# Optimization experiments

Hardware: AMD Instinct MI355X
Metric: run time of the kernel (lower is better)

The kernel has to match this reference:

```python
import jax, jax.numpy as jnp
import numpy as np
from jax.ops import segment_sum, segment_max

IN_CH, HID, OUT_CH, HEADS = 128, 64, 32, 4
N_NODES, N_EDGES = 50000, 800000
NEG_SLOPE = 0.2
EPS = 1e-16


def gat_layer(x, edge_index, W, att_src, att_dst, bias, heads, out_ch, concat):
    """PyG-style GATConv (add_self_loops=False, dropout=0, no edge features)."""
    N = x.shape[0]
    src, dst = edge_index[0], edge_index[1]
    h = (x @ W).reshape(N, heads, out_ch)                 # [N, H, C]
    a_src = jnp.einsum('nhc,hc->nh', h, att_src)          # [N, H]
    a_dst = jnp.einsum('nhc,hc->nh', h, att_dst)          # [N, H]
    e = jax.nn.leaky_relu(a_src[src] + a_dst[dst], NEG_SLOPE)  # [E, H]
    # segment softmax over incoming edges of each dst node
    m = segment_max(e, dst, num_segments=N)               # [N, H]
    ex = jnp.exp(e - m[dst])                              # [E, H]
    s = segment_sum(ex, dst, num_segments=N)              # [N, H]
    alpha = ex / (s[dst] + EPS)                           # [E, H]
    msg = h[src] * alpha[..., None]                       # [E, H, C]
    out = segment_sum(msg, dst, num_segments=N)           # [N, H, C]
    if concat:
        out = out.reshape(N, heads * out_ch)
    else:
        out = out.mean(axis=1)
    return out + bias, alpha


def setup_inputs() -> dict:
    key = jax.random.key(0)
    ks = jax.random.split(key, 10)
    s_in = 1.0 / np.sqrt(IN_CH)
    s_h = 1.0 / np.sqrt(HEADS * HID)
    return {
        'x': jax.random.normal(ks[0], (N_NODES, IN_CH), jnp.float32),
        'edge_index': jax.random.randint(ks[1], (2, N_EDGES), 0, N_NODES, jnp.int32),
        'W1': jax.random.normal(ks[2], (IN_CH, HEADS * HID), jnp.float32) * s_in,
        'att_src1': jax.random.normal(ks[3], (HEADS, HID), jnp.float32) * s_h,
        'att_dst1': jax.random.normal(ks[4], (HEADS, HID), jnp.float32) * s_h,
        'bias1': jnp.zeros((HEADS * HID,), jnp.float32),
        'W2': jax.random.normal(ks[5], (HEADS * HID, OUT_CH), jnp.float32) * s_h,
        'att_src2': jax.random.normal(ks[6], (1, OUT_CH), jnp.float32) * s_h,
        'att_dst2': jax.random.normal(ks[7], (1, OUT_CH), jnp.float32) * s_h,
        'bias2': jnp.zeros((OUT_CH,), jnp.float32),
    }


def reference(x, edge_index, W1, att_src1, att_dst1, bias1, W2, att_src2, att_dst2, bias2):
    h1, alpha1 = gat_layer(x, edge_index, W1, att_src1, att_dst1, bias1, HEADS, HID, concat=True)
    h1 = jax.nn.elu(h1)
    h2, alpha2 = gat_layer(h1, edge_index, W2, att_src2, att_dst2, bias2, 1, OUT_CH, concat=False)
    return h2, edge_index, alpha1, edge_index, alpha2
```

## Files before the change

### kernel.cpp

```cpp
#include <hip/hip_runtime.h>
#include <hip/hip_fp16.h>
#include <math.h>

#define NEG_SLOPE 0.2f
#define EPS_C 1e-16f

typedef _Float16 f16x8 __attribute__((ext_vector_type(8)));
typedef float f32x4 __attribute__((ext_vector_type(4)));

__device__ __forceinline__ float lrelu(float x){ return x > 0.f ? x : NEG_SLOPE * x; }
__device__ __forceinline__ float eluf(float x){ return x > 0.f ? x : expm1f(x); }

__global__ void zero_int_kernel(int* __restrict__ p, int n){
  int i = blockIdx.x * blockDim.x + threadIdx.x;
  if (i < n) p[i] = 0;
}

__global__ void count_deg_kernel(const int* __restrict__ dst, int* __restrict__ deg, int E){
  int i = blockIdx.x * blockDim.x + threadIdx.x;
  if (i < E) atomicAdd(&deg[dst[i]], 1);
}

__global__ __launch_bounds__(256) void scan1_kernel(const int* __restrict__ deg,
    int* __restrict__ offsets, int* __restrict__ blockSums, int N){
  __shared__ int sm[256];
  int b = blockIdx.x, t = threadIdx.x;
  int i = b * 256 + t;
  int v = (i < N) ? deg[i] : 0;
  sm[t] = v;
  __syncthreads();
  #pragma unroll
  for (int st = 1; st < 256; st <<= 1){
    int add = (t >= st) ? sm[t - st] : 0;
    __syncthreads();
    sm[t] += add;
    __syncthreads();
  }
  if (i < N) offsets[i] = sm[t] - v;
  if (t == 255) blockSums[b] = sm[255];
}

__global__ __launch_bounds__(256) void scan2_kernel(const int* __restrict__ blockSums,
    int* __restrict__ blockBase, int* __restrict__ offsetsN, int nb){
  __shared__ int sm[256];
  int t = threadIdx.x;
  int v = (t < nb) ? blockSums[t] : 0;
  sm[t] = v;
  __syncthreads();
  #pragma unroll
  for (int st = 1; st < 256; st <<= 1){
    int add = (t >= st) ? sm[t - st] : 0;
    __syncthreads();
    sm[t] += add;
    __syncthreads();
  }
  if (t < nb) blockBase[t] = sm[t] - v;
  if (t == 255) *offsetsN = sm[255];
}

__global__ __launch_bounds__(256) void scan3_kernel(int* __restrict__ offsets,
    const int* __restrict__ blockBase, int* __restrict__ cursor, int N){
  int b = blockIdx.x, t = threadIdx.x;
  int i = b * 256 + t;
  if (i < N){
    int v = offsets[i] + blockBase[b];
    offsets[i] = v;
    cursor[i] = v;
  }
}

__global__ void scatter_kernel(const int* __restrict__ src, const int* __restrict__ dst,
                               int* __restrict__ cursor, int* __restrict__ csr_src,
                               int* __restrict__ csr_eid, int E){
  int i = blockIdx.x * blockDim.x + threadIdx.x;
  if (i < E){
    int d = dst[i];
    int p = atomicAdd(&cursor[d], 1);
    csr_src[p] = src[i];
    csr_eid[p] = i;
  }
}

__global__ void cvt_x_kernel(const float* __restrict__ x, __half* __restrict__ x16, int n4){
  int i = blockIdx.x * blockDim.x + threadIdx.x;
  if (i < n4){
    float4 v = *reinterpret_cast<const float4*>(&x[(size_t)i * 4]);
    __half2 h01 = __floats2half2_rn(v.x, v.y);
    __half2 h23 = __floats2half2_rn(v.z, v.w);
    uint2 pack;
    pack.x = *reinterpret_cast<unsigned int*>(&h01);
    pack.y = *reinterpret_cast<unsigned int*>(&h23);
    *reinterpret_cast<uint2*>(&x16[(size_t)i * 4]) = pack;
  }
}

__global__ void cvt_w1_kernel(const float* __restrict__ W1, __half* __restrict__ W1t){
  int i = blockIdx.x * blockDim.x + threadIdx.x;
  int k = i >> 8, c = i & 255;
  if (i < 128 * 256) W1t[(size_t)c * 128 + k] = __float2half(W1[(size_t)k * 256 + c]);
}

__global__ __launch_bounds__(256) void gemm1_kernel(const __half* __restrict__ x16,
    const __half* __restrict__ W1t, const float* __restrict__ att_src,
    const float* __restrict__ att_dst, __half* __restrict__ h1,
    float* __restrict__ a_src_f, float* __restrict__ a_dst_f, int N){
  __shared__ _Float16 As[128 * 136];
  __shared__ _Float16 Bs[64 * 136];
  int tid = threadIdx.x;
  int lane = tid & 63, wid = tid >> 6;
  int rowBase = blockIdx.x * 128;
  int head = blockIdx.y;
  int colBase = head * 64;

  #pragma unroll
  for (int it = 0; it < 8; ++it){
    int li = it * 256 + tid;
    int r = li >> 4, seg = li & 15;
    int grow = rowBase + r;
    f16x8 v = {};
    if (grow < N) v = *reinterpret_cast<const f16x8*>(&x16[(size_t)grow * 128 + seg * 8]);
    *reinterpret_cast<f16x8*>(&As[r * 136 + seg * 8]) = v;
  }
  #pragma unroll
  for (int it = 0; it < 4; ++it){
    int li = it * 256 + tid;
    int c = li >> 4, seg = li & 15;
    f16x8 v = *reinterpret_cast<const f16x8*>(&W1t[(size_t)(colBase + c) * 128 + seg * 8]);
    *reinterpret_cast<f16x8*>(&Bs[c * 136 + seg * 8]) = v;
  }
  __syncthreads();

  f32x4 acc[2][4] = {};
  int l15 = lane & 15, l4 = lane >> 4;
  #pragma unroll
  for (int ks = 0; ks < 4; ++ks){
    int kOff = ks * 32 + l4 * 8;
    f16x8 a0 = *reinterpret_cast<const f16x8*>(&As[(wid * 32 + l15) * 136 + kOff]);
    f16x8 a1 = *reinterpret_cast<const f16x8*>(&As[(wid * 32 + 16 + l15) * 136 + kOff]);
    #pragma unroll
    for (int cc = 0; cc < 4; ++cc){
      f16x8 b = *reinterpret_cast<const f16x8*>(&Bs[(cc * 16 + l15) * 136 + kOff]);
      acc[0][cc] = __builtin_amdgcn_mfma_f32_16x16x32_f16(a0, b, acc[0][cc], 0, 0, 0);
      acc[1][cc] = __builtin_amdgcn_mfma_f32_16x16x32_f16(a1, b, acc[1][cc], 0, 0, 0);
    }
  }

  #pragma unroll
  for (int rr = 0; rr < 2; ++rr){
    #pragma unroll
    for (int i = 0; i < 4; ++i){
      int row = rowBase + wid * 32 + rr * 16 + l4 * 4 + i;
      if (row < N){
        #pragma unroll
        for (int cc = 0; cc < 4; ++cc)
          h1[(size_t)row * 256 + colBase + cc * 16 + l15] = __float2half(acc[rr][cc][i]);
      }
    }
  }
  float sw[4], dw[4];
  #pragma unroll
  for (int cc = 0; cc < 4; ++cc){
    sw[cc] = att_src[colBase + cc * 16 + l15];
    dw[cc] = att_dst[colBase + cc * 16 + l15];
  }
  #pragma unroll
  for (int rr = 0; rr < 2; ++rr){
    #pragma unroll
    for (int i = 0; i < 4; ++i){
      float ts = 0.f, td = 0.f;
      #pragma unroll
      for (int cc = 0; cc < 4; ++cc){
        ts += acc[rr][cc][i] * sw[cc];
        td += acc[rr][cc][i] * dw[cc];
      }
      #pragma unroll
      for (int st = 8; st > 0; st >>= 1){
        ts += __shfl_xor(ts, st);
        td += __shfl_xor(td, st);
      }
      int row = rowBase + wid * 32 + rr * 16 + l4 * 4 + i;
      if (l15 == 0 && row < N){
        a_src_f[(size_t)row * 4 + head] = ts;
        a_dst_f[(size_t)row * 4 + head] = td;
      }
    }
  }
}

__global__ __launch_bounds__(256) void node1_kernel(
    const __half* __restrict__ h1, const float4* __restrict__ a_src,
    const float* __restrict__ a_src_f, const float4* __restrict__ a_dst,
    const int* __restrict__ offsets, const int* __restrict__ csr_src,
    const int* __restrict__ csr_eid, const float* __restrict__ bias,
    float* __restrict__ h1b, float* __restrict__ alpha1_out, int N){
  int gid = blockIdx.x * blockDim.x + threadIdx.x;
  int n = gid >> 6, lane = gid & 63;
  if (n >= N) return;
  int off = offsets[n];
  int deg = offsets[n + 1] - off;
  float4 ad = a_dst[n];
  bool have0 = (lane < deg);
  float4 e0 = make_float4(-INFINITY, -INFINITY, -INFINITY, -INFINITY);
  if (have0){
    float4 as = a_src[csr_src[off + lane]];
    e0 = make_float4(lrelu(as.x + ad.x), lrelu(as.y + ad.y),
                     lrelu(as.z + ad.z), lrelu(as.w + ad.w));
  }
  float m0 = e0.x, m1 = e0.y, m2 = e0.z, m3 = e0.w;
  for (int i = lane + 64; i < deg; i += 64){
    float4 as = a_src[csr_src[off + i]];
    m0 = fmaxf(m0, lrelu(as.x + ad.x));
    m1 = fmaxf(m1, lrelu(as.y + ad.y));
    m2 = fmaxf(m2, lrelu(as.z + ad.z));
    m3 = fmaxf(m3, lrelu(as.w + ad.w));
  }
  #pragma unroll
  for (int st = 32; st > 0; st >>= 1){
    m0 = fmaxf(m0, __shfl_xor(m0, st));
    m1 = fmaxf(m1, __shfl_xor(m1, st));
    m2 = fmaxf(m2, __shfl_xor(m2, st));
    m3 = fmaxf(m3, __shfl_xor(m3, st));
  }
  float s0 = 0.f, s1 = 0.f, s2 = 0.f, s3 = 0.f;
  if (have0){
    s0 = __expf(e0.x - m0); s1 = __expf(e0.y - m1);
    s2 = __expf(e0.z - m2); s3 = __expf(e0.w - m3);
  }
  for (int i = lane + 64; i < deg; i += 64){
    float4 as = a_src[csr_src[off + i]];
    s0 += __expf(lrelu(as.x + ad.x) - m0);
    s1 += __expf(lrelu(as.y + ad.y) - m1);
    s2 += __expf(lrelu(as.z + ad.z) - m2);
    s3 += __expf(lrelu(as.w + ad.w) - m3);
  }
  #pragma unroll
  for (int st = 32; st > 0; st >>= 1){
    s0 += __shfl_xor(s0, st); s1 += __shfl_xor(s1, st);
    s2 += __shfl_xor(s2, st); s3 += __shfl_xor(s3, st);
  }
  float i0 = 1.f / (s0 + EPS_C), i1 = 1.f / (s1 + EPS_C);
  float i2 = 1.f / (s2 + EPS_C), i3 = 1.f / (s3 + EPS_C);
  if (have0){
    int eid = csr_eid[off + lane];
    *reinterpret_cast<float4*>(&alpha1_out[(size_t)eid * 4]) =
        make_float4(__expf(e0.x - m0) * i0, __expf(e0.y - m1) * i1,
                    __expf(e0.z - m2) * i2, __expf(e0.w - m3) * i3);
  }
  for (int i = lane + 64; i < deg; i += 64){
    int slot = off + i;
    float4 as = a_src[csr_src[slot]];
    int eid = csr_eid[slot];
    *reinterpret_cast<float4*>(&alpha1_out[(size_t)eid * 4]) =
        make_float4(__expf(lrelu(as.x + ad.x) - m0) * i0,
                    __expf(lrelu(as.y + ad.y) - m1) * i1,
                    __expf(lrelu(as.z + ad.z) - m2) * i2,
                    __expf(lrelu(as.w + ad.w) - m3) * i3);
  }
  int head = lane >> 4;
  float mh  = head == 0 ? m0 : head == 1 ? m1 : head == 2 ? m2 : m3;
  float ih  = head == 0 ? i0 : head == 1 ? i1 : head == 2 ? i2 : i3;
  float adh = head == 0 ? ad.x : head == 1 ? ad.y : head == 2 ? ad.z : ad.w;
  float4 accA = make_float4(0.f, 0.f, 0.f, 0.f);
  float4 accB = make_float4(0.f, 0.f, 0.f, 0.f);
  float4 accC = make_float4(0.f, 0.f, 0.f, 0.f);
  float4 accD = make_float4(0.f, 0.f, 0.f, 0.f);
  int j = 0;
  for (; j + 3 < deg; j += 4){
    int sA = csr_src[off + j];
    int sB = csr_src[off + j + 1];
    int sC = csr_src[off + j + 2];
    int sD = csr_src[off + j + 3];
    float alA = __expf(lrelu(a_src_f[(size_t)sA * 4 + head] + adh) - mh) * ih;
    float alB = __expf(lrelu(a_src_f[(size_t)sB * 4 + head] + adh) - mh) * ih;
    float alC = __expf(lrelu(a_src_f[(size_t)sC * 4 + head] + adh) - mh) * ih;
    float alD = __expf(lrelu(a_src_f[(size_t)sD * 4 + head] + adh) - mh) * ih;
    float2 rA = *reinterpret_cast<const float2*>(&h1[(size_t)sA * 256 + lane * 4]);
    float2 rB = *reinterpret_cast<const float2*>(&h1[(size_t)sB * 256 + lane * 4]);
    float2 rC = *reinterpret_cast<const float2*>(&h1[(size_t)sC * 256 + lane * 4]);
    float2 rD = *reinterpret_cast<const float2*>(&h1[(size_t)sD * 256 + lane * 4]);
    float2 fA0 = __half22float2(*reinterpret_cast<__half2*>(&rA.x));
    float2 fA1 = __half22float2(*reinterpret_cast<__half2*>(&rA.y));
    float2 fB0 = __half22float2(*reinterpret_cast<__half2*>(&rB.x));
    float2 fB1 = __half22float2(*reinterpret_cast<__half2*>(&rB.y));
    float2 fC0 = __half22float2(*reinterpret_cast<__half2*>(&rC.x));
    float2 fC1 = __half22float2(*reinterpret_cast<__half2*>(&rC.y));
    float2 fD0 = __half22float2(*reinterpret_cast<__half2*>(&rD.x));
    float2 fD1 = __half22float2(*reinterpret_cast<__half2*>(&rD.y));
    accA.x += alA * fA0.x; accA.y += alA * fA0.y; accA.z += alA * fA1.x; accA.w += alA * fA1.y;
    accB.x += alB * fB0.x; accB.y += alB * fB0.y; accB.z += alB * fB1.x; accB.w += alB * fB1.y;
    accC.x += alC * fC0.x; accC.y += alC * fC0.y; accC.z += alC * fC1.x; accC.w += alC * fC1.y;
    accD.x += alD * fD0.x; accD.y += alD * fD0.y; accD.z += alD * fD1.x; accD.w += alD * fD1.y;
  }
  for (; j < deg; ++j){
    int sA = csr_src[off + j];
    float alA = __expf(lrelu(a_src_f[(size_t)sA * 4 + head] + adh) - mh) * ih;
    float2 rA = *reinterpret_cast<const float2*>(&h1[(size_t)sA * 256 + lane * 4]);
    float2 fA0 = __half22float2(*reinterpret_cast<__half2*>(&rA.x));
    float2 fA1 = __half22float2(*reinterpret_cast<__half2*>(&rA.y));
    accA.x += alA * fA0.x; accA.y += alA * fA0.y; accA.z += alA * fA1.x; accA.w += alA * fA1.y;
  }
  accA.x += accB.x + accC.x + accD.x;
  accA.y += accB.y + accC.y + accD.y;
  accA.z += accB.z + accC.z + accD.z;
  accA.w += accB.w + accC.w + accD.w;
  float4 b = *reinterpret_cast<const float4*>(&bias[lane * 4]);
  float4 o = make_float4(eluf(accA.x + b.x), eluf(accA.y + b.y),
                         eluf(accA.z + b.z), eluf(accA.w + b.w));
  *reinterpret_cast<float4*>(&h1b[(size_t)n * 256 + lane * 4]) = o;
}

__global__ __launch_bounds__(256) void gemm2_kernel(const float* __restrict__ h1b,
    const float* __restrict__ W2, const float* __restrict__ att_src2,
    const float* __restrict__ att_dst2, float* __restrict__ h2pre,
    float* __restrict__ a_src2, float* __restrict__ a_dst2, int N){
  __shared__ float As[128][33];
  __shared__ float Bs[32][33];
  int tid = threadIdx.x;
  int tx = tid & 15, ty = tid >> 4;
  int rowBase = blockIdx.x * 128;
  float acc[8][2] = {};
  float4 pa[4], pb;

  #pragma unroll
  for (int it = 0; it < 4; ++it){
    int li = it * 256 + tid;
    int r = li >> 3, kk = (li & 7) << 2;
    int row = rowBase + r;
    pa[it] = (row < N) ? *reinterpret_cast<const float4*>(&h1b[(size_t)row * 256 + kk])
                       : make_float4(0.f, 0.f, 0.f, 0.f);
  }
  {
    int kr = tid >> 3, c4 = (tid & 7) << 2;
    pb = *reinterpret_cast<const float4*>(&W2[(size_t)kr * 32 + c4]);
  }
  #pragma unroll
  for (int it = 0; it < 4; ++it){
    int li = it * 256 + tid;
    int r = li >> 3, kk = (li & 7) << 2;
    As[r][kk] = pa[it].x; As[r][kk + 1] = pa[it].y;
    As[r][kk + 2] = pa[it].z; As[r][kk + 3] = pa[it].w;
  }
  {
    int kr = tid >> 3, c4 = (tid & 7) << 2;
    Bs[kr][c4] = pb.x; Bs[kr][c4 + 1] = pb.y; Bs[kr][c4 + 2] = pb.z; Bs[kr][c4 + 3] = pb.w;
  }
  __syncthreads();

  for (int k0 = 0; k0 < 256; k0 += 32){
    bool more = (k0 + 32) < 256;
    if (more){
      #pragma unroll
      for (int it = 0; it < 4; ++it){
        int li = it * 256 + tid;
        int r = li >> 3, kk = (li & 7) << 2;
        int row = rowBase + r;
        pa[it] = (row < N) ? *reinterpret_cast<const float4*>(&h1b[(size_t)row * 256 + k0 + 32 + kk])
                           : make_float4(0.f, 0.f, 0.f, 0.f);
      }
      int kr = tid >> 3, c4 = (tid & 7) << 2;
      pb = *reinterpret_cast<const float4*>(&W2[(size_t)(k0 + 32 + kr) * 32 + c4]);
    }
    #pragma unroll
    for (int kk = 0; kk < 32; ++kk){
      float b0 = Bs[kk][tx * 2], b1 = Bs[kk][tx * 2 + 1];
      #pragma unroll
      for (int j = 0; j < 8; ++j){
        float a = As[ty + 16 * j][kk];
        acc[j][0] += a * b0; acc[j][1] += a * b1;
      }
    }
    if (more){
      __syncthreads();
      #pragma unroll
      for (int it = 0; it < 4; ++it){
        int li = it * 256 + tid;
        int r = li >> 3, kk = (li & 7) << 2;
        As[r][kk] = pa[it].x; As[r][kk + 1] = pa[it].y;
        As[r][kk + 2] = pa[it].z; As[r][kk + 3] = pa[it].w;
      }
      int kr = tid >> 3, c4 = (tid & 7) << 2;
      Bs[kr][c4] = pb.x; Bs[kr][c4 + 1] = pb.y; Bs[kr][c4 + 2] = pb.z; Bs[kr][c4 + 3] = pb.w;
      __syncthreads();
    }
  }
  #pragma unroll
  for (int j = 0; j < 8; ++j){
    int row = rowBase + ty + 16 * j;
    if (row < N)
      *reinterpret_cast<float2*>(&h2pre[(size_t)row * 32 + tx * 2]) =
          make_float2(acc[j][0], acc[j][1]);
  }
  float s0 = att_src2[tx * 2], s1 = att_src2[tx * 2 + 1];
  float d0 = att_dst2[tx * 2], d1 = att_dst2[tx * 2 + 1];
  float ps[8], pd[8];
  #pragma unroll
  for (int j = 0; j < 8; ++j){
    ps[j] = acc[j][0] * s0 + acc[j][1] * s1;
    pd[j] = acc[j][0] * d0 + acc[j][1] * d1;
  }
  #pragma unroll
  for (int st = 8; st > 0; st >>= 1){
    #pragma unroll
    for (int j = 0; j < 8; ++j){
      ps[j] += __shfl_xor(ps[j], st);
      pd[j] += __shfl_xor(pd[j], st);
    }
  }
  if (tx == 0){
    #pragma unroll
    for (int j = 0; j < 8; ++j){
      int row = rowBase + ty + 16 * j;
      if (row < N){
        a_src2[row] = ps[j];
        a_dst2[row] = pd[j];
      }
    }
  }
}

__global__ __launch_bounds__(256) void node2_kernel(
    const float* __restrict__ h2pre, const float* __restrict__ a_src2,
    const float* __restrict__ a_dst2, const int* __restrict__ offsets,
    const int* __restrict__ csr_src, const int* __restrict__ csr_eid,
    const float* __restrict__ bias2, float* __restrict__ out_h2,
    float* __restrict__ alpha2_out, int N){
  int gid = blockIdx.x * blockDim.x + threadIdx.x;
  int n = gid >> 6, lane = gid & 63;
  if (n >= N) return;
  int off = offsets[n], deg = offsets[n + 1] - off;
  float adn = a_dst2[n];
  bool have0 = (lane < deg);
  float e0 = -INFINITY;
  if (have0) e0 = lrelu(a_src2[csr_src[off + lane]] + adn);
  float m = e0;
  for (int i = lane + 64; i < deg; i += 64)
    m = fmaxf(m, lrelu(a_src2[csr_src[off + i]] + adn));
  #pragma unroll
  for (int st = 32; st > 0; st >>= 1) m = fmaxf(m, __shfl_xor(m, st));
  float s = have0 ? __expf(e0 - m) : 0.f;
  for (int i = lane + 64; i < deg; i += 64)
    s += __expf(lrelu(a_src2[csr_src[off + i]] + adn) - m);
  #pragma unroll
  for (int st = 32; st > 0; st >>= 1) s += __shfl_xor(s, st);
  float inv = 1.f / (s + EPS_C);
  if (have0) alpha2_out[csr_eid[off + lane]] = __expf(e0 - m) * inv;
  for (int i = lane + 64; i < deg; i += 64){
    int slot = off + i;
    alpha2_out[csr_eid[slot]] = __expf(lrelu(a_src2[csr_src[slot]] + adn) - m) * inv;
  }
  int c = lane & 31, half = lane >> 5;
  float acc = 0.f;
  for (int j = half; j < deg; j += 2){
    int src = csr_src[off + j];
    float al = __expf(lrelu(a_src2[src] + adn) - m) * inv;
    acc += al * h2pre[(size_t)src * 32 + c];
  }
  acc += __shfl_xor(acc, 32);
  if (lane < 32) out_h2[(size_t)n * 32 + c] = acc + bias2[c];
}

__global__ void edge_out_kernel(const int* __restrict__ ei, float* __restrict__ out1,
                                float* __restrict__ out3, int n2e){
  int i = blockIdx.x * blockDim.x + threadIdx.x;
  if (i < n2e){
    float v = (float)ei[i];
    out1[i] = v; out3[i] = v;
  }
}

extern "C" void kernel_launch(void* const* d_in, const int* in_sizes, int n_in,
                              void* d_out, int out_size, void* d_ws, size_t ws_size,
                              hipStream_t stream){
  const float* x        = (const float*)d_in[0];
  const int*   ei       = (const int*)d_in[1];
  const float* W1       = (const float*)d_in[2];
  const float* att_src1 = (const float*)d_in[3];
  const float* att_dst1 = (const float*)d_in[4];
  const float* bias1    = (const float*)d_in[5];
  const float* W2       = (const float*)d_in[6];
  const float* att_src2 = (const float*)d_in[7];
  const float* att_dst2 = (const float*)d_in[8];
  const float* bias2    = (const float*)d_in[9];
  float* out = (float*)d_out;
  (void)n_in; (void)out_size; (void)ws_size;

  const int N = in_sizes[0] / 128;
  const int E = in_sizes[1] / 2;
  const int* src = ei;
  const int* dst = ei + E;
  const int nb = (N + 255) / 256;

  char* ws = (char*)d_ws;
  size_t o = 0;
  auto alloc = [&](size_t bytes) -> void* {
    void* p = ws + o;
    o += (bytes + 255) & ~(size_t)255;
    return p;
  };
  __half* h1      = (__half*)alloc((size_t)N * 256 * 2);
  __half* x16     = (__half*)alloc((size_t)N * 128 * 2);
  __half* W1t     = (__half*)alloc((size_t)256 * 128 * 2);
  float*  h1b     = (float*)alloc((size_t)N * 256 * 4);
  float*  h2pre   = (float*)alloc((size_t)N * 32 * 4);
  float*  a_src1  = (float*)alloc((size_t)N * 16);
  float*  a_dst1  = (float*)alloc((size_t)N * 16);
  float*  a_src2  = (float*)alloc((size_t)N * 4);
  float*  a_dst2  = (float*)alloc((size_t)N * 4);
  int*    deg     = (int*)alloc((size_t)N * 4);
  int*    offsets = (int*)alloc((size_t)(N + 1) * 4);
  int*    cursor  = (int*)alloc((size_t)N * 4);
  int*    csr_src = (int*)alloc((size_t)E * 4);
  int*    csr_eid = (int*)alloc((size_t)E * 4);
  int*    blockSums = (int*)alloc(256 * 4);
  int*    blockBase = (int*)alloc(256 * 4);

  const size_t OFF1 = (size_t)N * 32;
  const size_t OFF2 = OFF1 + (size_t)2 * E;
  const size_t OFF3 = OFF2 + (size_t)E * 4;
  const size_t OFF4 = OFF3 + (size_t)2 * E;

  int n4 = (N * 128) / 4;
  hipLaunchKernelGGL(cvt_x_kernel, dim3((n4 + 255) / 256), dim3(256), 0, stream, x, x16, n4);
  hipLaunchKernelGGL(cvt_w1_kernel, dim3(128), dim3(256), 0, stream, W1, W1t);
  hipLaunchKernelGGL(zero_int_kernel, dim3((N + 255) / 256), dim3(256), 0, stream, deg, N);
  hipLaunchKernelGGL(count_deg_kernel, dim3((E + 255) / 256), dim3(256), 0, stream, dst, deg, E);
  hipLaunchKernelGGL(scan1_kernel, dim3(nb), dim3(256), 0, stream, deg, offsets, blockSums, N);
  hipLaunchKernelGGL(scan2_kernel, dim3(1), dim3(256), 0, stream, blockSums, blockBase,
                     offsets + N, nb);
  hipLaunchKernelGGL(scan3_kernel, dim3(nb), dim3(256), 0, stream, offsets, blockBase, cursor, N);
  hipLaunchKernelGGL(scatter_kernel, dim3((E + 255) / 256), dim3(256), 0, stream,
                     src, dst, cursor, csr_src, csr_eid, E);
  hipLaunchKernelGGL(gemm1_kernel, dim3((N + 127) / 128, 4), dim3(256), 0, stream,
                     x16, W1t, att_src1, att_dst1, h1, a_src1, a_dst1, N);
  hipLaunchKernelGGL(node1_kernel, dim3((N * 64 + 255) / 256), dim3(256), 0, stream,
                     h1, (const float4*)a_src1, (const float*)a_src1, (const float4*)a_dst1,
                     offsets, csr_src, csr_eid, bias1, h1b, out + OFF2, N);
  hipLaunchKernelGGL(gemm2_kernel, dim3((N + 127) / 128), dim3(256), 0, stream,
                     h1b, W2, att_src2, att_dst2, h2pre, a_src2, a_dst2, N);
  hipLaunchKernelGGL(node2_kernel, dim3((N * 64 + 255) / 256), dim3(256), 0, stream,
                     h2pre, a_src2, a_dst2, offsets, csr_src, csr_eid, bias2,
                     out, out + OFF4, N);
  hipLaunchKernelGGL(edge_out_kernel, dim3((2 * E + 255) / 256), dim3(256), 0, stream,
                     ei, out + OFF1, out + OFF3, 2 * E);
}
```

Measured before the change: 389.9 us.

## Store layer-1 output in fp16, use MFMA for GEMM2, cache alphas in LDS

The post-ELU hidden activations and the second-layer projection are now stored as fp16 instead of fp32, halving their memory traffic. GEMM2 is rewritten around fp16 MFMA using a transposed fp16 copy of W2. Both node kernels keep the per-edge attention coefficients of the first 64 edges in LDS, so the aggregation loops no longer re-gather a_src and recompute the exponentials. The cost is reduced precision in the intermediate activations plus one extra tiny conversion kernel.

```diff
diff --git a/kernel.cpp b/kernel.cpp
--- a/kernel.cpp
+++ b/kernel.cpp
@@ -98,6 +98,12 @@
   int i = blockIdx.x * blockDim.x + threadIdx.x;
   int k = i >> 8, c = i & 255;
   if (i < 128 * 256) W1t[(size_t)c * 128 + k] = __float2half(W1[(size_t)k * 256 + c]);
+}
+
+__global__ void cvt_w2_kernel(const float* __restrict__ W2, __half* __restrict__ W2t){
+  int i = blockIdx.x * blockDim.x + threadIdx.x;
+  int k = i >> 5, c = i & 31;
+  if (i < 256 * 32) W2t[(size_t)c * 256 + k] = __float2half(W2[(size_t)k * 32 + c]);
 }
 
 __global__ __launch_bounds__(256) void gemm1_kernel(const __half* __restrict__ x16,
@@ -192,9 +198,10 @@
     const float* __restrict__ a_src_f, const float4* __restrict__ a_dst,
     const int* __restrict__ offsets, const int* __restrict__ csr_src,
     const int* __restrict__ csr_eid, const float* __restrict__ bias,
-    float* __restrict__ h1b, float* __restrict__ alpha1_out, int N){
+    __half* __restrict__ h1b, float* __restrict__ alpha1_out, int N){
+  __shared__ float al_lds[4][4][64];
   int gid = blockIdx.x * blockDim.x + threadIdx.x;
-  int n = gid >> 6, lane = gid & 63;
+  int n = gid >> 6, lane = gid & 63, wid = (threadIdx.x >> 6) & 3;
   if (n >= N) return;
   int off = offsets[n];
   int deg = offsets[n + 1] - off;
@@ -241,10 +248,12 @@
   float i0 = 1.f / (s0 + EPS_C), i1 = 1.f / (s1 + EPS_C);
   float i2 = 1.f / (s2 + EPS_C), i3 = 1.f / (s3 + EPS_C);
   if (have0){
+    float a0 = __expf(e0.x - m0) * i0, a1 = __expf(e0.y - m1) * i1;
+    float a2 = __expf(e0.z - m2) * i2, a3 = __expf(e0.w - m3) * i3;
+    al_lds[wid][0][lane] = a0; al_lds[wid][1][lane] = a1;
+    al_lds[wid][2][lane] = a2; al_lds[wid][3][lane] = a3;
     int eid = csr_eid[off + lane];
-    *reinterpret_cast<float4*>(&alpha1_out[(size_t)eid * 4]) =
-        make_float4(__expf(e0.x - m0) * i0, __expf(e0.y - m1) * i1,
-                    __expf(e0.z - m2) * i2, __expf(e0.w - m3) * i3);
+    *reinterpret_cast<float4*>(&alpha1_out[(size_t)eid * 4]) = make_float4(a0, a1, a2, a3);
   }
   for (int i = lane + 64; i < deg; i += 64){
     int slot = off + i;
@@ -264,16 +273,17 @@
   float4 accB = make_float4(0.f, 0.f, 0.f, 0.f);
   float4 accC = make_float4(0.f, 0.f, 0.f, 0.f);
   float4 accD = make_float4(0.f, 0.f, 0.f, 0.f);
+  int degL = deg < 64 ? deg : 64;
   int j = 0;
-  for (; j + 3 < deg; j += 4){
+  for (; j + 3 < degL; j += 4){
     int sA = csr_src[off + j];
     int sB = csr_src[off + j + 1];
     int sC = csr_src[off + j + 2];
     int sD = csr_src[off + j + 3];
-    float alA = __expf(lrelu(a_src_f[(size_t)sA * 4 + head] + adh) - mh) * ih;
-    float alB = __expf(lrelu(a_src_f[(size_t)sB * 4 + head] + adh) - mh) * ih;
-    float alC = __expf(lrelu(a_src_f[(size_t)sC * 4 + head] + adh) - mh) * ih;
-    float alD = __expf(lrelu(a_src_f[(size_t)sD * 4 + head] + adh) - mh) * ih;
+    float alA = al_lds[wid][head][j];
+    float alB = al_lds[wid][head][j + 1];
+    float alC = al_lds[wid][head][j + 2];
+    float alD = al_lds[wid][head][j + 3];
     float2 rA = *reinterpret_cast<const float2*>(&h1[(size_t)sA * 256 + lane * 4]);
     float2 rB = *reinterpret_cast<const float2*>(&h1[(size_t)sB * 256 + lane * 4]);
     float2 rC = *reinterpret_cast<const float2*>(&h1[(size_t)sC * 256 + lane * 4]);
@@ -291,6 +301,14 @@
     accC.x += alC * fC0.x; accC.y += alC * fC0.y; accC.z += alC * fC1.x; accC.w += alC * fC1.y;
     accD.x += alD * fD0.x; accD.y += alD * fD0.y; accD.z += alD * fD1.x; accD.w += alD * fD1.y;
   }
+  for (; j < degL; ++j){
+    int sA = csr_src[off + j];
+    float alA = al_lds[wid][head][j];
+    float2 rA = *reinterpret_cast<const float2*>(&h1[(size_t)sA * 256 + lane * 4]);
+    float2 fA0 = __half22float2(*reinterpret_cast<__half2*>(&rA.x));
+    float2 fA1 = __half22float2(*reinterpret_cast<__half2*>(&rA.y));
+    accA.x += alA * fA0.x; accA.y += alA * fA0.y; accA.z += alA * fA1.x; accA.w += alA * fA1.y;
+  }
   for (; j < deg; ++j){
     int sA = csr_src[off + j];
     float alA = __expf(lrelu(a_src_f[(size_t)sA * 4 + head] + adh) - mh) * ih;
@@ -304,128 +322,101 @@
   accA.z += accB.z + accC.z + accD.z;
   accA.w += accB.w + accC.w + accD.w;
   float4 b = *reinterpret_cast<const float4*>(&bias[lane * 4]);
-  float4 o = make_float4(eluf(accA.x + b.x), eluf(accA.y + b.y),
-                         eluf(accA.z + b.z), eluf(accA.w + b.w));
-  *reinterpret_cast<float4*>(&h1b[(size_t)n * 256 + lane * 4]) = o;
-}
-
-__global__ __launch_bounds__(256) void gemm2_kernel(const float* __restrict__ h1b,
-    const float* __restrict__ W2, const float* __restrict__ att_src2,
-    const float* __restrict__ att_dst2, float* __restrict__ h2pre,
+  __half2 o01 = __floats2half2_rn(eluf(accA.x + b.x), eluf(accA.y + b.y));
+  __half2 o23 = __floats2half2_rn(eluf(accA.z + b.z), eluf(accA.w + b.w));
+  uint2 pack;
+  pack.x = *reinterpret_cast<unsigned int*>(&o01);
+  pack.y = *reinterpret_cast<unsigned int*>(&o23);
+  *reinterpret_cast<uint2*>(&h1b[(size_t)n * 256 + lane * 4]) = pack;
+}
+
+__global__ __launch_bounds__(256) void gemm2_kernel(const __half* __restrict__ h1b,
+    const __half* __restrict__ W2t, const float* __restrict__ att_src2,
+    const float* __restrict__ att_dst2, __half* __restrict__ h2pre,
     float* __restrict__ a_src2, float* __restrict__ a_dst2, int N){
-  __shared__ float As[128][33];
-  __shared__ float Bs[32][33];
+  __shared__ _Float16 As[128 * 136];
+  __shared__ _Float16 Bs[32 * 136];
   int tid = threadIdx.x;
-  int tx = tid & 15, ty = tid >> 4;
+  int lane = tid & 63, wid = tid >> 6;
   int rowBase = blockIdx.x * 128;
-  float acc[8][2] = {};
-  float4 pa[4], pb;
-
-  #pragma unroll
-  for (int it = 0; it < 4; ++it){
-    int li = it * 256 + tid;
-    int r = li >> 3, kk = (li & 7) << 2;
-    int row = rowBase + r;
-    pa[it] = (row < N) ? *reinterpret_cast<const float4*>(&h1b[(size_t)row * 256 + kk])
-                       : make_float4(0.f, 0.f, 0.f, 0.f);
-  }
-  {
-    int kr = tid >> 3, c4 = (tid & 7) << 2;
-    pb = *reinterpret_cast<const float4*>(&W2[(size_t)kr * 32 + c4]);
-  }
-  #pragma unroll
-  for (int it = 0; it < 4; ++it){
-    int li = it * 256 + tid;
-    int r = li >> 3, kk = (li & 7) << 2;
-    As[r][kk] = pa[it].x; As[r][kk + 1] = pa[it].y;
-    As[r][kk + 2] = pa[it].z; As[r][kk + 3] = pa[it].w;
-  }
-  {
-    int kr = tid >> 3, c4 = (tid & 7) << 2;
-    Bs[kr][c4] = pb.x; Bs[kr][c4 + 1] = pb.y; Bs[kr][c4 + 2] = pb.z; Bs[kr][c4 + 3] = pb.w;
-  }
-  __syncthreads();
-
-  for (int k0 = 0; k0 < 256; k0 += 32){
-    bool more = (k0 + 32) < 256;
-    if (more){
+  int l15 = lane & 15, l4 = lane >> 4;
+  f32x4 acc[2][2] = {};
+
+  for (int kc = 0; kc < 2; ++kc){
+    if (kc) __syncthreads();
+    #pragma unroll
+    for (int it = 0; it < 8; ++it){
+      int li = it * 256 + tid;
+      int r = li >> 4, seg = li & 15;
+      int grow = rowBase + r;
+      f16x8 v = {};
+      if (grow < N) v = *reinterpret_cast<const f16x8*>(&h1b[(size_t)grow * 256 + kc * 128 + seg * 8]);
+      *reinterpret_cast<f16x8*>(&As[r * 136 + seg * 8]) = v;
+    }
+    #pragma unroll
+    for (int it = 0; it < 2; ++it){
+      int li = it * 256 + tid;
+      int c = li >> 4, seg = li & 15;
+      f16x8 v = *reinterpret_cast<const f16x8*>(&W2t[(size_t)c * 256 + kc * 128 + seg * 8]);
+      *reinterpret_cast<f16x8*>(&Bs[c * 136 + seg * 8]) = v;
+    }
+    __syncthreads();
+    #pragma unroll
+    for (int ks = 0; ks < 4; ++ks){
+      int kOff = ks * 32 + l4 * 8;
+      f16x8 a0 = *reinterpret_cast<const f16x8*>(&As[(wid * 32 + l15) * 136 + kOff]);
+      f16x8 a1 = *reinterpret_cast<const f16x8*>(&As[(wid * 32 + 16 + l15) * 136 + kOff]);
       #pragma unroll
-      for (int it = 0; it < 4; ++it){
-        int li = it * 256 + tid;
-        int r = li >> 3, kk = (li & 7) << 2;
-        int row = rowBase + r;
-        pa[it] = (row < N) ? *reinterpret_cast<const float4*>(&h1b[(size_t)row * 256 + k0 + 32 + kk])
-                           : make_float4(0.f, 0.f, 0.f, 0.f);
-      }
-      int kr = tid >> 3, c4 = (tid & 7) << 2;
-      pb = *reinterpret_cast<const float4*>(&W2[(size_t)(k0 + 32 + kr) * 32 + c4]);
-    }
-    #pragma unroll
-    for (int kk = 0; kk < 32; ++kk){
-      float b0 = Bs[kk][tx * 2], b1 = Bs[kk][tx * 2 + 1];
+      for (int cb = 0; cb < 2; ++cb){
+        f16x8 b = *reinterpret_cast<const f16x8*>(&Bs[(cb * 16 + l15) * 136 + kOff]);
+        acc[0][cb] = __builtin_amdgcn_mfma_f32_16x16x32_f16(a0, b, acc[0][cb], 0, 0, 0);
+        acc[1][cb] = __builtin_amdgcn_mfma_f32_16x16x32_f16(a1, b, acc[1][cb], 0, 0, 0);
+      }
+    }
+  }
+  #pragma unroll
+  for (int rr = 0; rr < 2; ++rr){
+    #pragma unroll
+    for (int i = 0; i < 4; ++i){
+      int row = rowBase + wid * 32 + rr * 16 + l4 * 4 + i;
+      if (row < N){
+        #pragma unroll
+        for (int cb = 0; cb < 2; ++cb)
+          h2pre[(size_t)row * 32 + cb * 16 + l15] = __float2half(acc[rr][cb][i]);
+      }
+    }
+  }
+  float sw0 = att_src2[l15], sw1 = att_src2[16 + l15];
+  float dw0 = att_dst2[l15], dw1 = att_dst2[16 + l15];
+  #pragma unroll
+  for (int rr = 0; rr < 2; ++rr){
+    #pragma unroll
+    for (int i = 0; i < 4; ++i){
+      float ts = acc[rr][0][i] * sw0 + acc[rr][1][i] * sw1;
+      float td = acc[rr][0][i] * dw0 + acc[rr][1][i] * dw1;
       #pragma unroll
-      for (int j = 0; j < 8; ++j){
-        float a = As[ty + 16 * j][kk];
-        acc[j][0] += a * b0; acc[j][1] += a * b1;
-      }
-    }
-    if (more){
-      __syncthreads();
-      #pragma unroll
-      for (int it = 0; it < 4; ++it){
-        int li = it * 256 + tid;
-        int r = li >> 3, kk = (li & 7) << 2;
-        As[r][kk] = pa[it].x; As[r][kk + 1] = pa[it].y;
-        As[r][kk + 2] = pa[it].z; As[r][kk + 3] = pa[it].w;
-      }
-      int kr = tid >> 3, c4 = (tid & 7) << 2;
-      Bs[kr][c4] = pb.x; Bs[kr][c4 + 1] = pb.y; Bs[kr][c4 + 2] = pb.z; Bs[kr][c4 + 3] = pb.w;
-      __syncthreads();
-    }
-  }
-  #pragma unroll
-  for (int j = 0; j < 8; ++j){
-    int row = rowBase + ty + 16 * j;
-    if (row < N)
-      *reinterpret_cast<float2*>(&h2pre[(size_t)row * 32 + tx * 2]) =
-          make_float2(acc[j][0], acc[j][1]);
-  }
-  float s0 = att_src2[tx * 2], s1 = att_src2[tx * 2 + 1];
-  float d0 = att_dst2[tx * 2], d1 = att_dst2[tx * 2 + 1];
-  float ps[8], pd[8];
-  #pragma unroll
-  for (int j = 0; j < 8; ++j){
-    ps[j] = acc[j][0] * s0 + acc[j][1] * s1;
-    pd[j] = acc[j][0] * d0 + acc[j][1] * d1;
-  }
-  #pragma unroll
-  for (int st = 8; st > 0; st >>= 1){
-    #pragma unroll
-    for (int j = 0; j < 8; ++j){
-      ps[j] += __shfl_xor(ps[j], st);
-      pd[j] += __shfl_xor(pd[j], st);
-    }
-  }
-  if (tx == 0){
-    #pragma unroll
-    for (int j = 0; j < 8; ++j){
-      int row = rowBase + ty + 16 * j;
-      if (row < N){
-        a_src2[row] = ps[j];
-        a_dst2[row] = pd[j];
+      for (int st = 8; st > 0; st >>= 1){
+        ts += __shfl_xor(ts, st);
+        td += __shfl_xor(td, st);
+      }
+      int row = rowBase + wid * 32 + rr * 16 + l4 * 4 + i;
+      if (l15 == 0 && row < N){
+        a_src2[row] = ts;
+        a_dst2[row] = td;
       }
     }
   }
 }
 
 __global__ __launch_bounds__(256) void node2_kernel(
-    const float* __restrict__ h2pre, const float* __restrict__ a_src2,
+    const __half* __restrict__ h2pre, const float* __restrict__ a_src2,
     const float* __restrict__ a_dst2, const int* __restrict__ offsets,
     const int* __restrict__ csr_src, const int* __restrict__ csr_eid,
     const float* __restrict__ bias2, float* __restrict__ out_h2,
     float* __restrict__ alpha2_out, int N){
+  __shared__ float al_lds[4][64];
   int gid = blockIdx.x * blockDim.x + threadIdx.x;
-  int n = gid >> 6, lane = gid & 63;
+  int n = gid >> 6, lane = gid & 63, wid = (threadIdx.x >> 6) & 3;
   if (n >= N) return;
   int off = offsets[n], deg = offsets[n + 1] - off;
   float adn = a_dst2[n];
@@ -443,17 +434,27 @@
   #pragma unroll
   for (int st = 32; st > 0; st >>= 1) s += __shfl_xor(s, st);
   float inv = 1.f / (s + EPS_C);
-  if (have0) alpha2_out[csr_eid[off + lane]] = __expf(e0 - m) * inv;
+  if (have0){
+    float al = __expf(e0 - m) * inv;
+    al_lds[wid][lane] = al;
+    alpha2_out[csr_eid[off + lane]] = al;
+  }
   for (int i = lane + 64; i < deg; i += 64){
     int slot = off + i;
     alpha2_out[csr_eid[slot]] = __expf(lrelu(a_src2[csr_src[slot]] + adn) - m) * inv;
   }
   int c = lane & 31, half = lane >> 5;
+  int degL = deg < 64 ? deg : 64;
   float acc = 0.f;
-  for (int j = half; j < deg; j += 2){
+  int j = half;
+  for (; j < degL; j += 2){
+    int src = csr_src[off + j];
+    acc += al_lds[wid][j] * __half2float(h2pre[(size_t)src * 32 + c]);
+  }
+  for (; j < deg; j += 2){
     int src = csr_src[off + j];
     float al = __expf(lrelu(a_src2[src] + adn) - m) * inv;
-    acc += al * h2pre[(size_t)src * 32 + c];
+    acc += al * __half2float(h2pre[(size_t)src * 32 + c]);
   }
   acc += __shfl_xor(acc, 32);
   if (lane < 32) out_h2[(size_t)n * 32 + c] = acc + bias2[c];
@@ -500,8 +501,9 @@
   __half* h1      = (__half*)alloc((size_t)N * 256 * 2);
   __half* x16     = (__half*)alloc((size_t)N * 128 * 2);
   __half* W1t     = (__half*)alloc((size_t)256 * 128 * 2);
-  float*  h1b     = (float*)alloc((size_t)N * 256 * 4);
-  float*  h2pre   = (float*)alloc((size_t)N * 32 * 4);
+  __half* W2t     = (__half*)alloc((size_t)32 * 256 * 2);
+  __half* h1b     = (__half*)alloc((size_t)N * 256 * 2);
+  __half* h2pre   = (__half*)alloc((size_t)N * 32 * 2);
   float*  a_src1  = (float*)alloc((size_t)N * 16);
   float*  a_dst1  = (float*)alloc((size_t)N * 16);
   float*  a_src2  = (float*)alloc((size_t)N * 4);
@@ -522,6 +524,7 @@
   int n4 = (N * 128) / 4;
   hipLaunchKernelGGL(cvt_x_kernel, dim3((n4 + 255) / 256), dim3(256), 0, stream, x, x16, n4);
   hipLaunchKernelGGL(cvt_w1_kernel, dim3(128), dim3(256), 0, stream, W1, W1t);
+  hipLaunchKernelGGL(cvt_w2_kernel, dim3(32), dim3(256), 0, stream, W2, W2t);
   hipLaunchKernelGGL(zero_int_kernel, dim3((N + 255) / 256), dim3(256), 0, stream, deg, N);
   hipLaunchKernelGGL(count_deg_kernel, dim3((E + 255) / 256), dim3(256), 0, stream, dst, deg, E);
   hipLaunchKernelGGL(scan1_kernel, dim3(nb), dim3(256), 0, stream, deg, offsets, blockSums, N);
@@ -536,7 +539,7 @@
                      h1, (const float4*)a_src1, (const float*)a_src1, (const float4*)a_dst1,
                      offsets, csr_src, csr_eid, bias1, h1b, out + OFF2, N);
   hipLaunchKernelGGL(gemm2_kernel, dim3((N + 127) / 128), dim3(256), 0, stream,
-                     h1b, W2, att_src2, att_dst2, h2pre, a_src2, a_dst2, N);
+                     h1b, W2t, att_src2, att_dst2, h2pre, a_src2, a_dst2, N);
   hipLaunchKernelGGL(node2_kernel, dim3((N * 64 + 255) / 256), dim3(256), 0, stream,
                      h2pre, a_src2, a_dst2, offsets, csr_src, csr_eid, bias2,
                      out, out + OFF4, N);
```

Result: faster. 361.4 us (-7.3%).
